# Kernel tuning notes

Measured on AMD Instinct MI355X. Metric: run time of the kernel, lower is better.

Reference implementation:

```python
import jax, jax.numpy as jnp
import numpy as np

D_MODEL = 1024
NUM_HEADS = 16
D_HEAD = 64
N_CTX = 2048
BATCH = 4
NEG_INF = -1e10  # matches torch masked_fill value


def setup_inputs() -> dict:
    key = jax.random.key(0)
    k1, k2, k3, k4, k5 = jax.random.split(key, 5)
    s = 1.0 / np.sqrt(D_MODEL).astype(np.float32)
    x = jax.random.normal(k1, (BATCH, N_CTX, D_MODEL), dtype=jnp.float32)
    W_K = jax.random.normal(k2, (NUM_HEADS, D_HEAD, D_MODEL), dtype=jnp.float32) * s
    W_Q = jax.random.normal(k3, (NUM_HEADS, D_HEAD, D_MODEL), dtype=jnp.float32) * s
    W_V = jax.random.normal(k4, (NUM_HEADS, D_HEAD, D_MODEL), dtype=jnp.float32) * s
    W_O = jax.random.normal(k5, (D_MODEL, NUM_HEADS * D_HEAD), dtype=jnp.float32) * s
    return {"x": x, "W_K": W_K, "W_Q": W_Q, "W_V": W_V, "W_O": W_O}


def reference(x, W_K, W_Q, W_V, W_O):
    b, q_len, d_model = x.shape
    d_head = W_K.shape[1]
    # projections: b=batch, p=pos, d=d_model, i=head, h=d_head
    K = jnp.einsum('bpd,ihd->biph', x, W_K)
    Q = jnp.einsum('bpd,ihd->biph', x, W_Q)
    V = jnp.einsum('bpd,ihd->biph', x, W_V)
    # scores[b, i, q, p] = Q[b,i,q,:] . K[b,i,p,:]
    scores = jnp.einsum('biph,biqh->biqp', K, Q)
    mask = jnp.tril(jnp.ones((q_len, q_len), dtype=bool))
    # NOTE: original masks with -1e10 BEFORE dividing by sqrt(d_head)
    scores = jnp.where(mask[None, None, :, :], scores, NEG_INF)
    attn = jax.nn.softmax(scores / np.sqrt(d_head).astype(np.float32), axis=-1)
    z = jnp.einsum('biph,biqp->biqh', V, attn)
    z_flat = jnp.transpose(z, (0, 2, 1, 3)).reshape(b, q_len, -1)  # b q (i h)
    out = jnp.einsum('bqf,df->bqd', z_flat, W_O)
    return out
```

## Files before the change

kernel.cpp:

```cpp
#include <hip/hip_runtime.h>
#include <hip/hip_bf16.h>


typedef short short8 __attribute__((ext_vector_type(8)));
typedef float f32x4 __attribute__((ext_vector_type(4)));

#define MFMA16(a, b, c) __builtin_amdgcn_mfma_f32_16x16x32_bf16((a), (b), (c), 0, 0, 0)

static __device__ __forceinline__ ushort f2bf(float f) {
  union { __hip_bfloat16 h; ushort u; } cv;
  cv.h = __float2bfloat16(f);
  return cv.u;
}

static __device__ __forceinline__ float fexp2(float x) {
#if __has_builtin(__builtin_amdgcn_exp2f)
  return __builtin_amdgcn_exp2f(x);
#else
  return __expf(x * 0.69314718056f);
#endif
}

static __device__ __forceinline__ void block_sync_lds() {
  asm volatile("s_waitcnt lgkmcnt(0)" ::: "memory");
  __builtin_amdgcn_s_barrier();
  __builtin_amdgcn_sched_barrier(0);
}

static __device__ __forceinline__ void block_sync_full() {
  asm volatile("s_waitcnt vmcnt(0) lgkmcnt(0)" ::: "memory");
  __builtin_amdgcn_s_barrier();
  __builtin_amdgcn_sched_barrier(0);
}

static __device__ __forceinline__ void store_out(float* p, float v) { *p = v; }
static __device__ __forceinline__ void store_out(__hip_bfloat16* p, float v) {
  *p = __float2bfloat16(v);
}

__global__ __launch_bounds__(256) void convert_all_kernel(
    const float* __restrict__ wq, const float* __restrict__ wk,
    const float* __restrict__ wv, const float* __restrict__ wo,
    const float* __restrict__ x, ushort* __restrict__ wqkv,
    ushort* __restrict__ wob, ushort* __restrict__ xb) {
  constexpr int W4 = 262144;
  constexpr size_t WSZ = (size_t)1024 * 1024;
  const int i = blockIdx.x * blockDim.x + threadIdx.x;
  const float* src;
  ushort* dst;
  int j;
  if (i < 2 * W4) {
    if (i < W4)      { src = wq; dst = wqkv;           j = i; }
    else             { src = wk; dst = wqkv + WSZ;     j = i - W4; }
  } else if (i < 4 * W4) {
    if (i < 3 * W4)  { src = wv; dst = wqkv + 2 * WSZ; j = i - 2 * W4; }
    else             { src = wo; dst = wob;            j = i - 3 * W4; }
  } else {
    src = x; dst = xb; j = i - 4 * W4;
  }
  const float4 v = ((const float4*)src)[j];
  ushort4 o;
  o.x = f2bf(v.x); o.y = f2bf(v.y); o.z = f2bf(v.z); o.w = f2bf(v.w);
  ((ushort4*)dst)[j] = o;
}

template <typename OUT_T>
__global__ __launch_bounds__(256, 2) void gemm_kernel(
    const ushort* __restrict__ A, int lda, const ushort* __restrict__ B, int ldb,
    OUT_T* __restrict__ C, int ldc, int K, int cpx) {
  __shared__ __align__(16) ushort As[2][128 * 64];
  __shared__ __align__(16) ushort Bs[2][128 * 64];
  const int tid = threadIdx.x;
  const int wave = tid >> 6, lane = tid & 63;
  const int lm = lane & 15, quad = lane >> 4;

  const int id = blockIdx.x;
  const int local = id >> 3;
  const int nt = (id & 7) * cpx + local % cpx;
  const int mt = local / cpx;
  const size_t m0 = (size_t)mt * 128;
  const size_t n0 = (size_t)nt * 128;

  const int rl = lane >> 3;
  const int cs = (lane & 7) ^ rl;
  const int fsw = lm & 7;
  const int wm = (wave >> 1) * 64, wn = (wave & 1) * 64;
  const int T = K >> 6;

#pragma unroll
  for (int j = 0; j < 4; ++j) {
    const int ch = wave * 4 + j;
    __builtin_amdgcn_global_load_lds(
        (const __attribute__((address_space(1))) void*)(B + (n0 + ch * 8 + rl) * (size_t)ldb + cs * 8),
        (__attribute__((address_space(3))) void*)(Bs[0] + ch * 512), 16, 0, 0);
    __builtin_amdgcn_global_load_lds(
        (const __attribute__((address_space(1))) void*)(A + (m0 + ch * 8 + rl) * (size_t)lda + cs * 8),
        (__attribute__((address_space(3))) void*)(As[0] + ch * 512), 16, 0, 0);
  }

  f32x4 acc[4][4] = {};
  for (int t = 0; t < T; ++t) {
    const int cur = t & 1;
    if (t + 1 < T) {
      const int k0 = (t + 1) << 6;
      ushort* an = As[cur ^ 1];
      ushort* bn = Bs[cur ^ 1];
#pragma unroll
      for (int j = 0; j < 4; ++j) {
        const int ch = wave * 4 + j;
        __builtin_amdgcn_global_load_lds(
            (const __attribute__((address_space(1))) void*)(B + (n0 + ch * 8 + rl) * (size_t)ldb + k0 + cs * 8),
            (__attribute__((address_space(3))) void*)(bn + ch * 512), 16, 0, 0);
        __builtin_amdgcn_global_load_lds(
            (const __attribute__((address_space(1))) void*)(A + (m0 + ch * 8 + rl) * (size_t)lda + k0 + cs * 8),
            (__attribute__((address_space(3))) void*)(an + ch * 512), 16, 0, 0);
      }
      asm volatile("s_waitcnt vmcnt(8)" ::: "memory");
    } else {
      asm volatile("s_waitcnt vmcnt(0)" ::: "memory");
    }
    __builtin_amdgcn_s_barrier();
    __builtin_amdgcn_sched_barrier(0);

    short8 a[4][2], b[4][2];
    const ushort* ab = As[cur];
    const ushort* bb = Bs[cur];
#pragma unroll
    for (int i = 0; i < 4; ++i) {
      const ushort* ar = ab + (wm + i * 16 + lm) * 64;
      const ushort* br = bb + (wn + i * 16 + lm) * 64;
#pragma unroll
      for (int ks = 0; ks < 2; ++ks) {
        const int off = (((ks * 4 + quad) ^ fsw) & 7) << 3;
        a[i][ks] = *(const short8*)(ar + off);
        b[i][ks] = *(const short8*)(br + off);
      }
    }
    asm volatile("s_waitcnt lgkmcnt(0)" ::: "memory");
    __builtin_amdgcn_s_barrier();
    __builtin_amdgcn_sched_barrier(0);

    __builtin_amdgcn_s_setprio(1);
#pragma unroll
    for (int i = 0; i < 4; ++i)
#pragma unroll
      for (int j = 0; j < 4; ++j)
#pragma unroll
        for (int ks = 0; ks < 2; ++ks)
          acc[i][j] = MFMA16(a[i][ks], b[j][ks], acc[i][j]);
    __builtin_amdgcn_s_setprio(0);
  }

  const int rq = quad * 4;
#pragma unroll
  for (int i = 0; i < 4; ++i)
#pragma unroll
    for (int j = 0; j < 4; ++j)
#pragma unroll
      for (int r = 0; r < 4; ++r)
        store_out(&C[(m0 + wm + i * 16 + rq + r) * (size_t)ldc + n0 + wn + j * 16 + lm],
                  acc[i][j][r]);
}

static __device__ __forceinline__ void stage_part(
    const ushort* __restrict__ Ab, int lda, const ushort* __restrict__ Bb,
    int ldb, int k0, ushort* abuf, ushort* bbuf, int wave, int lane, int part) {
  const int rl = lane >> 3, c8 = lane & 7;
  const int cs = c8 ^ rl;
  if (part == 0) {
#pragma unroll
    for (int i = 0; i < 2; ++i) {
      const int r = i * 64 + wave * 8 + rl;
      __builtin_amdgcn_global_load_lds(
          (const __attribute__((address_space(1))) void*)(Ab + (size_t)r * lda + k0 + cs * 8),
          (__attribute__((address_space(3))) void*)(abuf + (i * 8 + wave) * 512), 16, 0, 0);
    }
#pragma unroll
    for (int i = 0; i < 2; ++i) {
      const int r = i * 64 + wave * 8 + rl;
      __builtin_amdgcn_global_load_lds(
          (const __attribute__((address_space(1))) void*)(Bb + (size_t)r * ldb + k0 + cs * 8),
          (__attribute__((address_space(3))) void*)(bbuf + (i * 8 + wave) * 512), 16, 0, 0);
    }
  } else {
#pragma unroll
    for (int i = 2; i < 4; ++i) {
      const int r = i * 64 + wave * 8 + rl;
      __builtin_amdgcn_global_load_lds(
          (const __attribute__((address_space(1))) void*)(Bb + (size_t)r * ldb + k0 + cs * 8),
          (__attribute__((address_space(3))) void*)(bbuf + (i * 8 + wave) * 512), 16, 0, 0);
    }
  }
}

template <typename OUT_T>
__global__ __launch_bounds__(512, 2) void gemm3_kernel(
    const ushort* __restrict__ A, int lda, const ushort* __restrict__ B, int ldb,
    OUT_T* __restrict__ C, int ldc, int K) {
  __shared__ __align__(16) ushort As[3][128 * 64];
  __shared__ __align__(16) ushort Bs[3][256 * 64];

  const int tid = threadIdx.x;
  const int wave = tid >> 6, lane = tid & 63;
  const int lm = lane & 15, quad = lane >> 4;
  const int wm = wave >> 2, wn = wave & 3;

  const int id = blockIdx.x;
  const int mt = (id & 7) * 8 + ((id >> 3) & 7);
  const int nt = id >> 6;
  const size_t m0 = (size_t)mt * 128;
  const size_t n0 = (size_t)nt * 256;

  const ushort* Abase = A + m0 * (size_t)lda;
  const ushort* Bbase = B + n0 * (size_t)ldb;
  const int fsw = lm & 7;
  const int T = K >> 6;

  stage_part(Abase, lda, Bbase, ldb, 0, As[0], Bs[0], wave, lane, 0);
  stage_part(Abase, lda, Bbase, ldb, 0, As[0], Bs[0], wave, lane, 1);
  stage_part(Abase, lda, Bbase, ldb, 64, As[1], Bs[1], wave, lane, 0);
  stage_part(Abase, lda, Bbase, ldb, 64, As[1], Bs[1], wave, lane, 1);
  asm volatile("s_waitcnt vmcnt(6)" ::: "memory");
  __builtin_amdgcn_s_barrier();
  __builtin_amdgcn_sched_barrier(0);

  f32x4 acc[4][4] = {};
  int bt = 0, bs = 2;
  for (int t = 0; t < T; ++t) {
    const ushort* ab = As[bt];
    const ushort* bb = Bs[bt];
    const bool pre = (t + 2 < T);
    const int kp = (t + 2) << 6;

    short8 bfr[4][2], a0[2][2];
#pragma unroll
    for (int nf = 0; nf < 4; ++nf) {
      const ushort* br = bb + (wn * 64 + nf * 16 + lm) * 64;
#pragma unroll
      for (int ks = 0; ks < 2; ++ks)
        bfr[nf][ks] = *(const short8*)(br + ((((ks * 4 + quad) ^ fsw) & 7) << 3));
    }
#pragma unroll
    for (int mf = 0; mf < 2; ++mf) {
      const ushort* ar = ab + (wm * 64 + mf * 16 + lm) * 64;
#pragma unroll
      for (int ks = 0; ks < 2; ++ks)
        a0[mf][ks] = *(const short8*)(ar + ((((ks * 4 + quad) ^ fsw) & 7) << 3));
    }
    if (pre) stage_part(Abase, lda, Bbase, ldb, kp, As[bs], Bs[bs], wave, lane, 0);
    asm volatile("" ::: "memory");
    __builtin_amdgcn_s_barrier();
    asm volatile("s_waitcnt lgkmcnt(0)" ::: "memory");
    __builtin_amdgcn_sched_barrier(0);
    __builtin_amdgcn_s_setprio(1);
#pragma unroll
    for (int mf = 0; mf < 2; ++mf)
#pragma unroll
      for (int nf = 0; nf < 4; ++nf)
#pragma unroll
        for (int ks = 0; ks < 2; ++ks)
          acc[mf][nf] = MFMA16(a0[mf][ks], bfr[nf][ks], acc[mf][nf]);
    __builtin_amdgcn_s_setprio(0);
    asm volatile("" ::: "memory");
    __builtin_amdgcn_s_barrier();

    short8 a1[2][2];
#pragma unroll
    for (int mf = 0; mf < 2; ++mf) {
      const ushort* ar = ab + (wm * 64 + (mf + 2) * 16 + lm) * 64;
#pragma unroll
      for (int ks = 0; ks < 2; ++ks)
        a1[mf][ks] = *(const short8*)(ar + ((((ks * 4 + quad) ^ fsw) & 7) << 3));
    }
    if (pre) stage_part(Abase, lda, Bbase, ldb, kp, As[bs], Bs[bs], wave, lane, 1);
    if (pre) asm volatile("s_waitcnt vmcnt(6)" ::: "memory");
    else     asm volatile("s_waitcnt vmcnt(0)" ::: "memory");
    __builtin_amdgcn_s_barrier();
    asm volatile("s_waitcnt lgkmcnt(0)" ::: "memory");
    __builtin_amdgcn_sched_barrier(0);
    __builtin_amdgcn_s_setprio(1);
#pragma unroll
    for (int mf = 0; mf < 2; ++mf)
#pragma unroll
      for (int nf = 0; nf < 4; ++nf)
#pragma unroll
        for (int ks = 0; ks < 2; ++ks)
          acc[mf + 2][nf] = MFMA16(a1[mf][ks], bfr[nf][ks], acc[mf + 2][nf]);
    __builtin_amdgcn_s_setprio(0);
    asm volatile("" ::: "memory");
    __builtin_amdgcn_s_barrier();

    bt = (bt == 2) ? 0 : bt + 1;
    bs = (bs == 2) ? 0 : bs + 1;
  }

#pragma unroll
  for (int mf = 0; mf < 4; ++mf)
#pragma unroll
    for (int nf = 0; nf < 4; ++nf)
#pragma unroll
      for (int r = 0; r < 4; ++r)
        store_out(&C[(m0 + wm * 64 + mf * 16 + quad * 4 + r) * (size_t)ldc +
                     n0 + wn * 64 + nf * 16 + lm],
                  acc[mf][nf][r]);
}

static __device__ __forceinline__ void vt_write8(ushort* vtbuf, int h0, int hsw,
                                                 int p, const short8& v) {
  const int pc = (p >> 3) ^ hsw;
  ushort* row = vtbuf + h0 * 64 + (p & 7);
#pragma unroll
  for (int u = 0; u < 8; ++u)
    row[u * 64 + (((pc ^ u) & 7) << 3)] = ((const ushort*)&v)[u];
}

static __device__ __forceinline__ void stage_k(const ushort* kglob, int pbase,
                                               ushort* kbuf, int wave, int lane) {
  const int rl = lane >> 3;
  const int c = (lane & 7) ^ rl;
#pragma unroll
  for (int j = 0; j < 2; ++j) {
    const int ch = wave * 2 + j;
    const ushort* src = kglob + (size_t)(pbase + ch * 8 + rl) * 3072 + c * 8;
    __builtin_amdgcn_global_load_lds(
        (const __attribute__((address_space(1))) void*)src,
        (__attribute__((address_space(3))) void*)(kbuf + ch * 512), 16, 0, 0);
  }
}

__global__ __launch_bounds__(256) void flash4_kernel(ushort* __restrict__ QKV) {
  constexpr int LD = 3072;
  __shared__ __align__(16) ushort vt[2][64 * 64];
  __shared__ __align__(16) ushort kt[2][64 * 64];
  __shared__ __align__(16) ushort pbuf[4][16 * 64];

  const int id = blockIdx.x;
  const int g = (id & 7) * 8 + ((id >> 3) & 7);
  const int m = id >> 6;
  const int head = g & 15;
  const int b = g >> 4;

  const int tid = threadIdx.x;
  const int wave = tid >> 6, lane = tid & 63;
  const int lm = lane & 15, quad = lane >> 4;

  const size_t qcol = (size_t)b * 2048 * LD + head * 64;
  const size_t vcol = qcol + 2048;
  const ushort* kglob = QKV + qcol + 1024;

  const int h0 = (tid & 7) * 8;
  const int hsw = tid & 7;
  const int plb = tid >> 3;
  const int psw = lm & 7;
  const int ksw = lm & 7;

  constexpr float CSC = 0.180336880f;
  const short8 vone = {0x3F80, 0x3F80, 0x3F80, 0x3F80,
                       0x3F80, 0x3F80, 0x3F80, 0x3F80};

  for (int pass = 0; pass < 2; ++pass) {
    const int qbi = pass ? 31 - m : m;
    const int qrow = qbi * 64 + wave * 16;
    const int qg = qrow + lm;
    const int nt = qbi + 1;

    const ushort* qp = QKV + qcol + (size_t)(qrow + lm) * LD;
    short8 qa0 = *(const short8*)(qp + quad * 8);
    short8 qa1 = *(const short8*)(qp + 32 + quad * 8);

    f32x4 accz[4] = {};
    f32x4 lacc = {};

    block_sync_lds();

    stage_k(kglob, 0, kt[0], wave, lane);
#pragma unroll
    for (int rr = 0; rr < 2; ++rr) {
      const int p = plb + rr * 32;
      short8 v = *(const short8*)(QKV + vcol + (size_t)p * LD + h0);
      vt_write8(vt[0], h0, hsw, p, v);
    }

    for (int it = 0; it < nt; ++it) {
      const int p0 = it * 64;
      block_sync_full();

      short8 ka[4], kb[4];
      const ushort* kbuf = kt[it & 1];
#pragma unroll
      for (int s = 0; s < 4; ++s) {
        const ushort* kr = kbuf + (s * 16 + lm) * 64;
        ka[s] = *(const short8*)(kr + (((quad ^ ksw) & 7) << 3));
        kb[s] = *(const short8*)(kr + ((((quad + 4) ^ ksw) & 7) << 3));
      }

      const bool more = (it + 1 < nt);
      short8 nv0, nv1;
      if (more) {
        nv0 = *(const short8*)(QKV + vcol + (size_t)(p0 + 64 + plb) * LD + h0);
        nv1 = *(const short8*)(QKV + vcol + (size_t)(p0 + 96 + plb) * LD + h0);
        stage_k(kglob, p0 + 64, kt[(it + 1) & 1], wave, lane);
      }

      f32x4 t4[4];
      __builtin_amdgcn_s_setprio(1);
#pragma unroll
      for (int s = 0; s < 4; ++s) {
        f32x4 t = {0.f, 0.f, 0.f, 0.f};
        t = MFMA16(ka[s], qa0, t);
        t = MFMA16(kb[s], qa1, t);
        t4[s] = t;
      }
      __builtin_amdgcn_s_setprio(0);

      float ps[4][4];
      if (it != nt - 1) {
#pragma unroll
        for (int s = 0; s < 4; ++s)
#pragma unroll
          for (int r = 0; r < 4; ++r)
            ps[s][r] = fexp2(t4[s][r] * CSC);
      } else {
#pragma unroll
        for (int s = 0; s < 4; ++s)
#pragma unroll
          for (int r = 0; r < 4; ++r) {
            const int pg = p0 + s * 16 + quad * 4 + r;
            const float e = fexp2(t4[s][r] * CSC);
            ps[s][r] = (pg > qg) ? 0.f : e;
          }
      }

      ushort* pw = pbuf[wave] + lm * 64;
#pragma unroll
      for (int s = 0; s < 4; ++s) {
        uint2 pk;
        pk.x = (uint)f2bf(ps[s][0]) | ((uint)f2bf(ps[s][1]) << 16);
        pk.y = (uint)f2bf(ps[s][2]) | ((uint)f2bf(ps[s][3]) << 16);
        *(uint2*)(pw + ((((2 * s + (quad >> 1)) ^ psw) & 7) << 3) +
                  ((quad & 1) << 2)) = pk;
      }

      const ushort* vbuf = vt[it & 1];
      __builtin_amdgcn_s_setprio(1);
#pragma unroll
      for (int kc = 0; kc < 2; ++kc) {
        short8 pa = *(const short8*)(pw + ((((kc * 4 + quad) ^ psw) & 7) << 3));
        lacc = MFMA16(pa, vone, lacc);
#pragma unroll
        for (int c = 0; c < 4; ++c) {
          const int hrow = c * 16 + lm;
          const int fh = ((hrow >> 3) ^ hrow) & 7;
          short8 vb = *(const short8*)(
              vbuf + hrow * 64 + ((((4 * kc + quad) ^ fh) & 7) << 3));
          accz[c] = MFMA16(pa, vb, accz[c]);
        }
      }
      __builtin_amdgcn_s_setprio(0);

      if (more) {
        ushort* nbuf = vt[(it + 1) & 1];
        vt_write8(nbuf, h0, hsw, plb, nv0);
        vt_write8(nbuf, h0, hsw, plb + 32, nv1);
      }
    }

#pragma unroll
    for (int r = 0; r < 4; ++r) {
      const float inv = 1.f / lacc[r];
#pragma unroll
      for (int c = 0; c < 4; ++c)
        QKV[qcol + (size_t)(qrow + quad * 4 + r) * LD + c * 16 + lm] =
            f2bf(accz[c][r] * inv);
    }
  }
}

extern "C" void kernel_launch(void* const* d_in, const int* in_sizes, int n_in,
                              void* d_out, int out_size, void* d_ws, size_t ws_size,
                              hipStream_t stream) {
  (void)in_sizes; (void)n_in; (void)out_size; (void)ws_size;
  const float* x  = (const float*)d_in[0];
  const float* wk = (const float*)d_in[1];
  const float* wq = (const float*)d_in[2];
  const float* wv = (const float*)d_in[3];
  const float* wo = (const float*)d_in[4];
  float* out = (float*)d_out;

  const size_t WSZ = (size_t)1024 * 1024;
  ushort* wqkv_b = (ushort*)d_ws;
  ushort* wo_b = wqkv_b + 3 * WSZ;
  ushort* QKV = wo_b + WSZ;
  ushort* xb = (ushort*)d_out;

  convert_all_kernel<<<12288, 256, 0, stream>>>(wq, wk, wv, wo, x,
                                                wqkv_b, wo_b, xb);

  gemm3_kernel<__hip_bfloat16><<<768, 512, 0, stream>>>(
      xb, 1024, wqkv_b, 1024, (__hip_bfloat16*)QKV, 3072, 1024);

  flash4_kernel<<<1024, 256, 0, stream>>>(QKV);

  gemm_kernel<float><<<512, 256, 0, stream>>>(
      QKV, 3072, wo_b, 1024, out, 1024, 1024, 1);
}
```

Baseline: 253.8 us.

## Split QKV GEMM main loop into four quadrant phases interleaving LDS reads and MFMA

Restructures the QKV projection GEMM inner loop from two phases into four 2x2-fragment quadrant phases. Each phase loads only the A/B fragments it needs from LDS, then runs a small MFMA block, so LDS reads overlap earlier MFMAs and fewer fragment registers are live at once. Global-to-LDS staging is spread across the phases. The cost is more barriers per iteration and smaller MFMA bursts, which may reduce issue efficiency.

```diff
diff --git a/kernel.cpp b/kernel.cpp
--- a/kernel.cpp
+++ b/kernel.cpp
@@ -193,8 +193,14 @@
   }
 }
 
+static __device__ __forceinline__ void phase_sync() {
+  __builtin_amdgcn_s_barrier();
+  asm volatile("s_waitcnt lgkmcnt(0)" ::: "memory");
+  __builtin_amdgcn_sched_barrier(0);
+}
+
 template <typename OUT_T>
-__global__ __launch_bounds__(512, 2) void gemm3_kernel(
+__global__ __launch_bounds__(512, 2) void gemm8p_kernel(
     const ushort* __restrict__ A, int lda, const ushort* __restrict__ B, int ldb,
     OUT_T* __restrict__ C, int ldc, int K) {
   __shared__ __align__(16) ushort As[3][128 * 64];
@@ -232,63 +238,84 @@
     const bool pre = (t + 2 < T);
     const int kp = (t + 2) << 6;
 
-    short8 bfr[4][2], a0[2][2];
-#pragma unroll
-    for (int nf = 0; nf < 4; ++nf) {
-      const ushort* br = bb + (wn * 64 + nf * 16 + lm) * 64;
+    short8 a01[2][2], a23[2][2], b01[2][2], b23[2][2];
+
+#pragma unroll
+    for (int f = 0; f < 2; ++f) {
+      const ushort* ar = ab + (wm * 64 + f * 16 + lm) * 64;
+      const ushort* br = bb + (wn * 64 + f * 16 + lm) * 64;
+#pragma unroll
+      for (int ks = 0; ks < 2; ++ks) {
+        const int off = (((ks * 4 + quad) ^ fsw) & 7) << 3;
+        a01[f][ks] = *(const short8*)(ar + off);
+        b01[f][ks] = *(const short8*)(br + off);
+      }
+    }
+    if (pre) stage_part(Abase, lda, Bbase, ldb, kp, As[bs], Bs[bs], wave, lane, 0);
+    phase_sync();
+    __builtin_amdgcn_s_setprio(1);
+#pragma unroll
+    for (int mf = 0; mf < 2; ++mf)
+#pragma unroll
+      for (int nf = 0; nf < 2; ++nf)
+#pragma unroll
+        for (int ks = 0; ks < 2; ++ks)
+          acc[mf][nf] = MFMA16(a01[mf][ks], b01[nf][ks], acc[mf][nf]);
+    __builtin_amdgcn_s_setprio(0);
+
+#pragma unroll
+    for (int f = 0; f < 2; ++f) {
+      const ushort* br = bb + (wn * 64 + (f + 2) * 16 + lm) * 64;
 #pragma unroll
       for (int ks = 0; ks < 2; ++ks)
-        bfr[nf][ks] = *(const short8*)(br + ((((ks * 4 + quad) ^ fsw) & 7) << 3));
-    }
-#pragma unroll
-    for (int mf = 0; mf < 2; ++mf) {
-      const ushort* ar = ab + (wm * 64 + mf * 16 + lm) * 64;
+        b23[f][ks] = *(const short8*)(br + ((((ks * 4 + quad) ^ fsw) & 7) << 3));
+    }
+    phase_sync();
+    __builtin_amdgcn_s_setprio(1);
+#pragma unroll
+    for (int mf = 0; mf < 2; ++mf)
+#pragma unroll
+      for (int nf = 0; nf < 2; ++nf)
+#pragma unroll
+        for (int ks = 0; ks < 2; ++ks)
+          acc[mf][nf + 2] = MFMA16(a01[mf][ks], b23[nf][ks], acc[mf][nf + 2]);
+    __builtin_amdgcn_s_setprio(0);
+
+#pragma unroll
+    for (int f = 0; f < 2; ++f) {
+      const ushort* ar = ab + (wm * 64 + (f + 2) * 16 + lm) * 64;
 #pragma unroll
       for (int ks = 0; ks < 2; ++ks)
-        a0[mf][ks] = *(const short8*)(ar + ((((ks * 4 + quad) ^ fsw) & 7) << 3));
-    }
-    if (pre) stage_part(Abase, lda, Bbase, ldb, kp, As[bs], Bs[bs], wave, lane, 0);
-    asm volatile("" ::: "memory");
+        a23[f][ks] = *(const short8*)(ar + ((((ks * 4 + quad) ^ fsw) & 7) << 3));
+    }
+    if (pre) stage_part(Abase, lda, Bbase, ldb, kp, As[bs], Bs[bs], wave, lane, 1);
+    phase_sync();
+    __builtin_amdgcn_s_setprio(1);
+#pragma unroll
+    for (int mf = 0; mf < 2; ++mf)
+#pragma unroll
+      for (int nf = 0; nf < 2; ++nf)
+#pragma unroll
+        for (int ks = 0; ks < 2; ++ks)
+          acc[mf + 2][nf] = MFMA16(a23[mf][ks], b01[nf][ks], acc[mf + 2][nf]);
+    __builtin_amdgcn_s_setprio(0);
+
     __builtin_amdgcn_s_barrier();
-    asm volatile("s_waitcnt lgkmcnt(0)" ::: "memory");
     __builtin_amdgcn_sched_barrier(0);
     __builtin_amdgcn_s_setprio(1);
 #pragma unroll
     for (int mf = 0; mf < 2; ++mf)
 #pragma unroll
-      for (int nf = 0; nf < 4; ++nf)
+      for (int nf = 0; nf < 2; ++nf)
 #pragma unroll
         for (int ks = 0; ks < 2; ++ks)
-          acc[mf][nf] = MFMA16(a0[mf][ks], bfr[nf][ks], acc[mf][nf]);
+          acc[mf + 2][nf + 2] = MFMA16(a23[mf][ks], b23[nf][ks], acc[mf + 2][nf + 2]);
     __builtin_amdgcn_s_setprio(0);
-    asm volatile("" ::: "memory");
-    __builtin_amdgcn_s_barrier();
-
-    short8 a1[2][2];
-#pragma unroll
-    for (int mf = 0; mf < 2; ++mf) {
-      const ushort* ar = ab + (wm * 64 + (mf + 2) * 16 + lm) * 64;
-#pragma unroll
-      for (int ks = 0; ks < 2; ++ks)
-        a1[mf][ks] = *(const short8*)(ar + ((((ks * 4 + quad) ^ fsw) & 7) << 3));
-    }
-    if (pre) stage_part(Abase, lda, Bbase, ldb, kp, As[bs], Bs[bs], wave, lane, 1);
+
     if (pre) asm volatile("s_waitcnt vmcnt(6)" ::: "memory");
     else     asm volatile("s_waitcnt vmcnt(0)" ::: "memory");
     __builtin_amdgcn_s_barrier();
-    asm volatile("s_waitcnt lgkmcnt(0)" ::: "memory");
     __builtin_amdgcn_sched_barrier(0);
-    __builtin_amdgcn_s_setprio(1);
-#pragma unroll
-    for (int mf = 0; mf < 2; ++mf)
-#pragma unroll
-      for (int nf = 0; nf < 4; ++nf)
-#pragma unroll
-        for (int ks = 0; ks < 2; ++ks)
-          acc[mf + 2][nf] = MFMA16(a1[mf][ks], bfr[nf][ks], acc[mf + 2][nf]);
-    __builtin_amdgcn_s_setprio(0);
-    asm volatile("" ::: "memory");
-    __builtin_amdgcn_s_barrier();
 
     bt = (bt == 2) ? 0 : bt + 1;
     bs = (bs == 2) ? 0 : bs + 1;
@@ -496,7 +523,7 @@
   convert_all_kernel<<<12288, 256, 0, stream>>>(wq, wk, wv, wo, x,
                                                 wqkv_b, wo_b, xb);
 
-  gemm3_kernel<__hip_bfloat16><<<768, 512, 0, stream>>>(
+  gemm8p_kernel<__hip_bfloat16><<<768, 512, 0, stream>>>(
       xb, 1024, wqkv_b, 1024, (__hip_bfloat16*)QKV, 3072, 1024);
 
   flash4_kernel<<<1024, 256, 0, stream>>>(QKV);
```

New measurement: 258.7 us. No clear change (+2.0%).
